# Optimization experiments

Hardware: AMD Instinct MI355X
Metric: run time of the kernel (lower is better)

## Reference

```python
import jax, jax.numpy as jnp
import numpy as np

B, S, D, H = 2, 2048, 1024, 16
HD = D // H  # 64


def setup_inputs() -> dict:
    key = jax.random.key(0)
    ks = jax.random.split(key, 11)
    w_scale = 1.0 / np.sqrt(D)
    Q = jax.random.normal(ks[0], (B, S, D), jnp.float32)
    K = jax.random.normal(ks[1], (B, S, D), jnp.float32)
    V = jax.random.normal(ks[2], (B, S, D), jnp.float32)
    # causal mask: True = masked (matches torch masked_fill semantics)
    mask = ~jnp.tril(jnp.ones((S, S), bool))[None, None]  # [1,1,S,S]
    # RoPE freqs (precomputed cos/sin of freqs_cis, shape [S, HD//2])
    inv_freq = 1.0 / (10000.0 ** (jnp.arange(0, HD, 2, dtype=jnp.float32) / HD))
    angles = jnp.arange(S, dtype=jnp.float32)[:, None] * inv_freq[None, :]
    freqs_cos, freqs_sin = jnp.cos(angles), jnp.sin(angles)
    wq = jax.random.normal(ks[3], (D, D), jnp.float32) * w_scale
    wk = jax.random.normal(ks[4], (D, D), jnp.float32) * w_scale
    wv = jax.random.normal(ks[5], (D, D), jnp.float32) * w_scale
    wo = jax.random.normal(ks[6], (D, D), jnp.float32) * w_scale
    bq = jax.random.normal(ks[7], (D,), jnp.float32) * 0.01
    bk = jax.random.normal(ks[8], (D,), jnp.float32) * 0.01
    bv = jax.random.normal(ks[9], (D,), jnp.float32) * 0.01
    bo = jax.random.normal(ks[10], (D,), jnp.float32) * 0.01
    return {"Q": Q, "K": K, "V": V, "mask": mask,
            "freqs_cos": freqs_cos, "freqs_sin": freqs_sin,
            "wq": wq, "bq": bq, "wk": wk, "bk": bk,
            "wv": wv, "bv": bv, "wo": wo, "bo": bo}


def _rope(x, cos, sin):
    # x: [B,S,H,HD]; complex pairing of adjacent dims as in view_as_complex
    xr, xi = x[..., 0::2], x[..., 1::2]
    c = cos[None, :, None, :]
    s = sin[None, :, None, :]
    out_r = xr * c - xi * s
    out_i = xr * s + xi * c
    return jnp.stack([out_r, out_i], axis=-1).reshape(x.shape)


def reference(Q, K, V, mask, freqs_cos, freqs_sin, wq, bq, wk, bk, wv, bv, wo, bo):
    b, s, d = Q.shape
    h = H
    hd = d // h
    q = (Q @ wq.T + bq).reshape(b, s, h, hd)
    k = (K @ wk.T + bk).reshape(b, s, h, hd)
    v = (V @ wv.T + bv).reshape(b, s, h, hd)
    q = _rope(q, freqs_cos, freqs_sin)
    k = _rope(k, freqs_cos, freqs_sin)
    q = q.transpose(0, 2, 1, 3)  # [B,H,S,HD]
    k = k.transpose(0, 2, 1, 3)
    v = v.transpose(0, 2, 1, 3)
    scale = jnp.sqrt(jnp.float32(hd))
    energy = jnp.einsum('bhqd,bhkd->bhqk', q, k) / scale
    energy = jnp.where(mask, jnp.float32(-1e10), energy)
    attn = jax.nn.softmax(energy, axis=-1)  # dropout p=0.0 -> identity
    out = jnp.einsum('bhqk,bhkd->bhqd', attn, v)
    out = out.transpose(0, 2, 1, 3).reshape(b, s, d)
    return out @ wo.T + bo
```

## Files before the change

### kernel.cpp

```cpp
#include <hip/hip_runtime.h>
#include <stdint.h>

#define NB 2
#define NS 2048
#define ND 1024
#define NH 16
#define NHD 64
#define NM (NB*NS)

typedef __bf16 bf16;
typedef float f32x4 __attribute__((ext_vector_type(4)));
typedef __bf16 bf16x8 __attribute__((ext_vector_type(8)));
typedef __bf16 bf16x4 __attribute__((ext_vector_type(4)));

#define MFMA16(a,b,c) __builtin_amdgcn_mfma_f32_16x16x32_bf16(a,b,c,0,0,0)

__device__ __forceinline__ void gld_lds16(const bf16* g, bf16* l) {
  __builtin_amdgcn_global_load_lds((const __attribute__((address_space(1))) void*)g,
                                   (__attribute__((address_space(3))) void*)l,
                                   16, 0, 0);
}

__device__ __forceinline__ void block_sync_lds() {
  asm volatile("s_waitcnt lgkmcnt(0)\n\ts_barrier" ::: "memory");
}

__global__ __launch_bounds__(256)
void cvt3(const float* __restrict__ s0, const float* __restrict__ s1,
          const float* __restrict__ s2, bf16* __restrict__ dst, int n4each) {
  const int t = blockIdx.y;
  const float* s = (t == 0) ? s0 : (t == 1) ? s1 : s2;
  int i = blockIdx.x * blockDim.x + threadIdx.x;
  if (i >= n4each) return;
  float4 v = ((const float4*)s)[i];
  bf16x4 o = { (bf16)v.x, (bf16)v.y, (bf16)v.z, (bf16)v.w };
  ((bf16x4*)(dst + (size_t)t * n4each * 4))[i] = o;
}

__global__ __launch_bounds__(256)
void cvt_w4(const float* __restrict__ s0, const float* __restrict__ s1,
            const float* __restrict__ s2, const float* __restrict__ s3,
            bf16* __restrict__ dst, int n4each) {
  const int t = blockIdx.y;
  const float* s = (t == 0) ? s0 : (t == 1) ? s1 : (t == 2) ? s2 : s3;
  int i = blockIdx.x * blockDim.x + threadIdx.x;
  if (i >= n4each) return;
  float4 v = ((const float4*)s)[i];
  bf16x4 o = { (bf16)v.x, (bf16)v.y, (bf16)v.z, (bf16)v.w };
  ((bf16x4*)(dst + (size_t)t * n4each * 4))[i] = o;
}

template<int MODE>
__global__ __launch_bounds__(256)
void gemm_nt(const bf16* __restrict__ A, const bf16* __restrict__ W,
             const float* __restrict__ b0, const float* __restrict__ b1,
             const float* __restrict__ b2,
             const float* __restrict__ fc, const float* __restrict__ fs,
             bf16* __restrict__ obf, float* __restrict__ of) {
  constexpr int K = ND;
  __shared__ __align__(16) bf16 As[128 * 32];
  __shared__ __align__(16) bf16 Bs[128 * 32];
  const int tid = threadIdx.x;
  const int w = tid >> 6, lane = tid & 63;
  const int nt = blockIdx.x, mt = blockIdx.y, t = blockIdx.z;
  const bf16* Ab = A + (size_t)t * ((size_t)NM * K);
  const bf16* Wb = W + (size_t)t * ((size_t)ND * K);
  const float* bias = (t == 0) ? b0 : (t == 1) ? b1 : b2;
  const int wr = (w >> 1) * 64, wc = (w & 1) * 64;
  f32x4 acc[4][4] = {};
  const bf16* ga = Ab + (size_t)(mt * 128 + (tid >> 2)) * K + (tid & 3) * 8;
  const bf16* gb = Wb + (size_t)(nt * 128 + (tid >> 2)) * K + (tid & 3) * 8;
  bf16* lA = As + w * 512;
  bf16* lB = Bs + w * 512;
  for (int k0 = 0; k0 < K; k0 += 32) {
    __syncthreads();
    gld_lds16(ga + k0, lA);
    gld_lds16(ga + (size_t)64 * K + k0, lA + 64 * 32);
    gld_lds16(gb + k0, lB);
    gld_lds16(gb + (size_t)64 * K + k0, lB + 64 * 32);
    __syncthreads();
    bf16x8 af[4], bfr[4];
#pragma unroll
    for (int i = 0; i < 4; ++i) {
      af[i]  = *(const bf16x8*)&As[(wr + i * 16 + (lane & 15)) * 32 + (lane >> 4) * 8];
      bfr[i] = *(const bf16x8*)&Bs[(wc + i * 16 + (lane & 15)) * 32 + (lane >> 4) * 8];
    }
#pragma unroll
    for (int i = 0; i < 4; ++i)
#pragma unroll
      for (int j = 0; j < 4; ++j)
        acc[i][j] = MFMA16(af[i], bfr[j], acc[i][j]);
  }
#pragma unroll
  for (int i = 0; i < 4; ++i) {
#pragma unroll
    for (int j = 0; j < 4; ++j) {
      const int gcol = nt * 128 + wc + j * 16 + (lane & 15);
      const float bv = bias[gcol];
#pragma unroll
      for (int r = 0; r < 4; ++r) {
        const int grow = mt * 128 + wr + i * 16 + (lane >> 4) * 4 + r;
        float v = acc[i][j][r] + bv;
        if (MODE == 0) {
          const int b = grow >> 11, s = grow & (NS - 1);
          const int h = gcol >> 6, hd = gcol & 63;
          if (t < 2) {
            float pv = __shfl_xor(v, 1);
            const int ii = hd >> 1;
            float c  = fc[(s << 5) + ii];
            float sn = fs[(s << 5) + ii];
            v = ((hd & 1) == 0) ? (v * c - pv * sn) : (pv * sn + v * c);
            if (t == 0) v *= 0.18033688011112042f;
          }
          obf[(size_t)t * ((size_t)NM * ND) +
              (((size_t)(b * NH + h) * NS + s) * NHD + hd)] = (bf16)v;
        } else {
          of[(size_t)grow * ND + gcol] = v;
        }
      }
    }
  }
}

__global__ __launch_bounds__(256)
void transpose_v(const bf16* __restrict__ v, bf16* __restrict__ vt) {
  __shared__ __align__(16) bf16 t[64][72];
  const int s0 = blockIdx.x * 64;
  const int bh = blockIdx.y;
  const bf16* src = v + ((size_t)bh * NS + s0) * NHD;
#pragma unroll
  for (int it = 0; it < 2; ++it) {
    int slot = threadIdx.x + it * 256;
    int r = slot >> 3, c8 = (slot & 7) * 8;
    *(bf16x8*)&t[r][c8] = *(const bf16x8*)&src[(size_t)r * NHD + c8];
  }
  __syncthreads();
  bf16* dst = vt + (size_t)bh * NHD * NS + s0;
#pragma unroll
  for (int it = 0; it < 2; ++it) {
    int slot = threadIdx.x + it * 256;
    int r = slot >> 3, c8 = (slot & 7) * 8;
    bf16x8 vv;
#pragma unroll
    for (int e = 0; e < 8; ++e) vv[e] = t[c8 + e][r];
    *(bf16x8*)&dst[(size_t)r * NS + c8] = vv;
  }
}

__device__ __forceinline__ void attn_tile(
    const bf16 (*__restrict__ Ksh)[72], const bf16 (*__restrict__ Vsh)[72],
    bf16 (*__restrict__ Pw)[72], const bf16x8* qf, f32x4* o,
    float& m, float& l, int qi, int kk0, bool diag, int qrow, int grp) {
  f32x4 sc[4] = {};
  __builtin_amdgcn_s_setprio(1);
#pragma unroll
  for (int ch = 0; ch < 2; ++ch)
#pragma unroll
    for (int cb = 0; cb < 4; ++cb) {
      bf16x8 kf = *(const bf16x8*)&Ksh[cb * 16 + qrow][ch * 32 + grp * 8];
      sc[cb] = MFMA16(kf, qf[ch], sc[cb]);
    }
  __builtin_amdgcn_s_setprio(0);

  if (diag) {
#pragma unroll
    for (int cb = 0; cb < 4; ++cb)
#pragma unroll
      for (int r = 0; r < 4; ++r)
        if (kk0 + cb * 16 + grp * 4 + r > qi) sc[cb][r] = -1e30f;
  }

  float pm = sc[0][0];
#pragma unroll
  for (int cb = 0; cb < 4; ++cb)
#pragma unroll
    for (int r = 0; r < 4; ++r) pm = fmaxf(pm, sc[cb][r]);
  pm = fmaxf(pm, __shfl_xor(pm, 16));
  pm = fmaxf(pm, __shfl_xor(pm, 32));
  const float mn = fmaxf(m, pm);
  const float scl = exp2f(m - mn);
  m = mn;
  l *= scl;
#pragma unroll
  for (int cb = 0; cb < 4; ++cb) {
    bf16x4 pk;
#pragma unroll
    for (int r = 0; r < 4; ++r) {
      float p = exp2f(sc[cb][r] - mn);
      l += p;
      pk[r] = (bf16)p;
    }
    *(bf16x4*)&Pw[qrow][cb * 16 + grp * 4] = pk;
  }
#pragma unroll
  for (int hb = 0; hb < 4; ++hb)
#pragma unroll
    for (int r = 0; r < 4; ++r) o[hb][r] *= scl;

  __builtin_amdgcn_s_setprio(1);
#pragma unroll
  for (int ch = 0; ch < 2; ++ch) {
    bf16x8 pa = *(const bf16x8*)&Pw[qrow][ch * 32 + grp * 8];
#pragma unroll
    for (int hb = 0; hb < 4; ++hb) {
      bf16x8 vf = *(const bf16x8*)&Vsh[hb * 16 + qrow][ch * 32 + grp * 8];
      o[hb] = MFMA16(vf, pa, o[hb]);
    }
  }
  __builtin_amdgcn_s_setprio(0);
}

__global__ __launch_bounds__(512, 4)
void attn_k(const bf16* __restrict__ q, const bf16* __restrict__ k,
            const bf16* __restrict__ vt, bf16* __restrict__ out) {
  __shared__ __align__(16) char smem[55296];
  auto Ks = (bf16(*)[64][72])smem;
  auto Vs = (bf16(*)[64][72])(smem + 18432);
  auto P  = (bf16(*)[16][72])(smem + 36864);
  auto MO = (float(*)[2][16][68])smem;
  auto ML = (float(*)[2][16][2])(smem + 36864);

  const int tid = threadIdx.x;
  const int w = tid >> 6, lane = tid & 63;
  const int h = w >> 2, wl = w & 3;
  const int qrow = lane & 15, grp = lane >> 4;
  const int bh = blockIdx.x, j = blockIdx.y;
  const int b = bh >> 4, hh = bh & (NH - 1);
  const int tA = j, tB = 31 - j;

  const bf16* qb = q + (size_t)bh * NS * NHD;
  const bf16* kb = k + (size_t)bh * NS * NHD;
  const bf16* vb = vt + (size_t)bh * NHD * NS;

  const int nA = (j >= h) ? (((j - h) >> 1) + 1) : 0;
  const int nB = (((31 - j) - h) >> 1) + 1;
  const int len = nA + nB;

  const int q0A = tA * 64 + wl * 16, q0B = tB * 64 + wl * 16;
  bf16x8 qfA[2], qfB[2];
#pragma unroll
  for (int ch = 0; ch < 2; ++ch) {
    qfA[ch] = *(const bf16x8*)&qb[(size_t)(q0A + qrow) * NHD + ch * 32 + grp * 8];
    qfB[ch] = *(const bf16x8*)&qb[(size_t)(q0B + qrow) * NHD + ch * 32 + grp * 8];
  }

  f32x4 oA[4] = {}, oB[4] = {};
  float mA = -1e30f, lA = 0.f, mB = -1e30f, lB = 0.f;

  const int local = tid & 255;
  const int r0 = local >> 3, c0 = (local & 7) * 8;

  bf16x8 ka0, ka1, va0, va1;
  auto load_round = [&](int r) {
    const bool isA = r < nA;
    const int kt = isA ? (h + 2 * r) : (h + 2 * (r - nA));
    const int kk0 = kt * 64;
    ka0 = *(const bf16x8*)&kb[(size_t)(kk0 + r0) * NHD + c0];
    ka1 = *(const bf16x8*)&kb[(size_t)(kk0 + r0 + 32) * NHD + c0];
    va0 = *(const bf16x8*)&vb[(size_t)r0 * NS + kk0 + c0];
    va1 = *(const bf16x8*)&vb[(size_t)(r0 + 32) * NS + kk0 + c0];
  };

  load_round(0);
  for (int r = 0; r < 17; ++r) {
    const bool act = r < len;
    if (act) {
      *(bf16x8*)&Ks[h][r0][c0]      = ka0;
      *(bf16x8*)&Ks[h][r0 + 32][c0] = ka1;
      *(bf16x8*)&Vs[h][r0][c0]      = va0;
      *(bf16x8*)&Vs[h][r0 + 32][c0] = va1;
    }
    block_sync_lds();
    const bool isA = r < nA;
    const int kt = isA ? (h + 2 * r) : (h + 2 * (r - nA));
    if (r + 1 < len) load_round(r + 1);
    if (act) {
      if (isA)
        attn_tile(Ks[h], Vs[h], P[w], qfA, oA, mA, lA,
                  q0A + qrow, kt * 64, kt == tA, qrow, grp);
      else
        attn_tile(Ks[h], Vs[h], P[w], qfB, oB, mB, lB,
                  q0B + qrow, kt * 64, kt == tB, qrow, grp);
    }
    block_sync_lds();
  }

  lA += __shfl_xor(lA, 16); lA += __shfl_xor(lA, 32);
  lB += __shfl_xor(lB, 16); lB += __shfl_xor(lB, 32);

  __syncthreads();

  if (h == 1) {
#pragma unroll
    for (int hb = 0; hb < 4; ++hb) {
      *(f32x4*)&MO[wl][0][qrow][hb * 16 + grp * 4] = oA[hb];
      *(f32x4*)&MO[wl][1][qrow][hb * 16 + grp * 4] = oB[hb];
    }
    if (grp == 0) {
      ML[wl][0][qrow][0] = mA; ML[wl][0][qrow][1] = lA;
      ML[wl][1][qrow][0] = mB; ML[wl][1][qrow][1] = lB;
    }
  }
  __syncthreads();

  if (h == 0) {
#pragma unroll
    for (int sub = 0; sub < 2; ++sub) {
      const float m0 = sub ? mB : mA, l0 = sub ? lB : lA;
      const f32x4* o0 = sub ? oB : oA;
      const float m1 = ML[wl][sub][qrow][0], l1 = ML[wl][sub][qrow][1];
      const float mm = fmaxf(m0, m1);
      const float s0 = exp2f(m0 - mm), s1 = exp2f(m1 - mm);
      const float inv = 1.f / (l0 * s0 + l1 * s1);
      const int s = (sub ? q0B : q0A) + qrow;
      bf16* op = out + (size_t)(b * NS + s) * ND + hh * NHD + grp * 4;
#pragma unroll
      for (int hb = 0; hb < 4; ++hb) {
        f32x4 o1 = *(const f32x4*)&MO[wl][sub][qrow][hb * 16 + grp * 4];
        bf16x4 ov = { (bf16)((o0[hb][0] * s0 + o1[0] * s1) * inv),
                      (bf16)((o0[hb][1] * s0 + o1[1] * s1) * inv),
                      (bf16)((o0[hb][2] * s0 + o1[2] * s1) * inv),
                      (bf16)((o0[hb][3] * s0 + o1[3] * s1) * inv) };
        *(bf16x4*)&op[hb * 16] = ov;
      }
    }
  }
}

extern "C" void kernel_launch(void* const* d_in, const int* in_sizes, int n_in,
                              void* d_out, int out_size, void* d_ws, size_t ws_size,
                              hipStream_t stream) {
  const float* Q  = (const float*)d_in[0];
  const float* K  = (const float*)d_in[1];
  const float* V  = (const float*)d_in[2];
  const float* fc = (const float*)d_in[4];
  const float* fs = (const float*)d_in[5];
  const float* wq = (const float*)d_in[6];
  const float* bq = (const float*)d_in[7];
  const float* wk = (const float*)d_in[8];
  const float* bk = (const float*)d_in[9];
  const float* wv = (const float*)d_in[10];
  const float* bv = (const float*)d_in[11];
  const float* wo = (const float*)d_in[12];
  const float* bo = (const float*)d_in[13];
  float* out = (float*)d_out;
  bf16* ws = (bf16*)d_ws;

  const size_t MB_ = 1024 * 1024;
  bf16* Qbf  = ws;
  bf16* Wqkv = ws + 12 * MB_;
  bf16* Wo   = ws + 15 * MB_;
  bf16* qp   = ws + 16 * MB_;
  bf16* kp   = ws + 20 * MB_;
  bf16* vp   = ws + 24 * MB_;
  bf16* vtp  = ws + 28 * MB_;
  bf16* aout = ws + 32 * MB_;

  cvt3<<<dim3(4096, 3), 256, 0, stream>>>(Q, K, V, Qbf, 1048576);
  cvt_w4<<<dim3(1024, 4), 256, 0, stream>>>(wq, wk, wv, wo, Wqkv, 262144);

  gemm_nt<0><<<dim3(8, 32, 3), 256, 0, stream>>>(Qbf, Wqkv, bq, bk, bv, fc, fs, qp, nullptr);

  transpose_v<<<dim3(32, 32), 256, 0, stream>>>(vp, vtp);

  attn_k<<<dim3(32, 16), 512, 0, stream>>>(qp, kp, vtp, aout);

  gemm_nt<1><<<dim3(8, 32, 1), 256, 0, stream>>>(aout, Wo, bo, bo, bo, fc, fs, nullptr, out);
}
```

Before: 144.1 us.

## Double-buffer GEMM LDS loads, remap blocks per XCD, narrow output-projection tile

The GEMM kernel now double-buffers its LDS tiles and issues the next k-slice's global-to-LDS loads before computing the current one. Partial vmcnt waits let memory traffic overlap the MFMA work. Blocks are launched on a 1D grid and remapped so that consecutive IDs on the same XCD share M-tiles, which is meant to improve L2 reuse. The output projection uses a 64-wide N tile, giving 512 blocks instead of 256 to fill more CUs, at the cost of doubled LDS use and fewer MFMAs per load.

```diff
diff --git a/kernel.cpp b/kernel.cpp
--- a/kernel.cpp
+++ b/kernel.cpp
@@ -58,49 +58,80 @@
              const float* __restrict__ fc, const float* __restrict__ fs,
              bf16* __restrict__ obf, float* __restrict__ of) {
   constexpr int K = ND;
-  __shared__ __align__(16) bf16 As[128 * 32];
-  __shared__ __align__(16) bf16 Bs[128 * 32];
+  constexpr int BN = (MODE == 0) ? 128 : 64;
+  constexpr int NJ = (MODE == 0) ? 4 : 2;
+  __shared__ __align__(16) bf16 As[2][128 * 32];
+  __shared__ __align__(16) bf16 Bs[2][BN * 32];
   const int tid = threadIdx.x;
   const int w = tid >> 6, lane = tid & 63;
-  const int nt = blockIdx.x, mt = blockIdx.y, t = blockIdx.z;
+
+  const int id = blockIdx.x;
+  const int xcd = id & 7, r = id >> 3;
+  int t, nt, mt;
+  if (MODE == 0) { t = r >> 5; const int rem = r & 31; nt = rem & 7;  mt = xcd + 8 * (rem >> 3); }
+  else           { t = 0;                              nt = r & 15;   mt = xcd + 8 * (r >> 4);   }
+
   const bf16* Ab = A + (size_t)t * ((size_t)NM * K);
   const bf16* Wb = W + (size_t)t * ((size_t)ND * K);
   const float* bias = (t == 0) ? b0 : (t == 1) ? b1 : b2;
-  const int wr = (w >> 1) * 64, wc = (w & 1) * 64;
-  f32x4 acc[4][4] = {};
+  const int wr = (w >> 1) * 64, wc = (w & 1) * (BN / 2);
+  f32x4 acc[4][NJ] = {};
   const bf16* ga = Ab + (size_t)(mt * 128 + (tid >> 2)) * K + (tid & 3) * 8;
-  const bf16* gb = Wb + (size_t)(nt * 128 + (tid >> 2)) * K + (tid & 3) * 8;
-  bf16* lA = As + w * 512;
-  bf16* lB = Bs + w * 512;
+  const bf16* gb = Wb + (size_t)(nt * BN + (tid >> 2)) * K + (tid & 3) * 8;
+  bf16* lA = (bf16*)As + w * 512;
+  bf16* lB = (bf16*)Bs + w * 512;
+
+  auto issue = [&](int k0, int buf) {
+    gld_lds16(ga + k0, lA + buf * (128 * 32));
+    gld_lds16(ga + (size_t)64 * K + k0, lA + buf * (128 * 32) + 64 * 32);
+    if (MODE == 0) {
+      gld_lds16(gb + k0, lB + buf * (BN * 32));
+      gld_lds16(gb + (size_t)64 * K + k0, lB + buf * (BN * 32) + 64 * 32);
+    } else {
+      gld_lds16(gb + k0, lB + buf * (BN * 32));
+    }
+  };
+
+  issue(0, 0);
+  int cur = 0;
   for (int k0 = 0; k0 < K; k0 += 32) {
-    __syncthreads();
-    gld_lds16(ga + k0, lA);
-    gld_lds16(ga + (size_t)64 * K + k0, lA + 64 * 32);
-    gld_lds16(gb + k0, lB);
-    gld_lds16(gb + (size_t)64 * K + k0, lB + 64 * 32);
-    __syncthreads();
-    bf16x8 af[4], bfr[4];
-#pragma unroll
-    for (int i = 0; i < 4; ++i) {
-      af[i]  = *(const bf16x8*)&As[(wr + i * 16 + (lane & 15)) * 32 + (lane >> 4) * 8];
-      bfr[i] = *(const bf16x8*)&Bs[(wc + i * 16 + (lane & 15)) * 32 + (lane >> 4) * 8];
-    }
+    const bool last = (k0 + 32 >= K);
+    if (!last) {
+      issue(k0 + 32, cur ^ 1);
+      if (MODE == 0) asm volatile("s_waitcnt vmcnt(4)" ::: "memory");
+      else           asm volatile("s_waitcnt vmcnt(3)" ::: "memory");
+    } else {
+      asm volatile("s_waitcnt vmcnt(0)" ::: "memory");
+    }
+    __builtin_amdgcn_s_barrier();
+
+    bf16x8 af[4], bfr[NJ];
 #pragma unroll
     for (int i = 0; i < 4; ++i)
-#pragma unroll
-      for (int j = 0; j < 4; ++j)
+      af[i] = *(const bf16x8*)&As[cur][(wr + i * 16 + (lane & 15)) * 32 + (lane >> 4) * 8];
+#pragma unroll
+    for (int j = 0; j < NJ; ++j)
+      bfr[j] = *(const bf16x8*)&Bs[cur][(wc + j * 16 + (lane & 15)) * 32 + (lane >> 4) * 8];
+#pragma unroll
+    for (int i = 0; i < 4; ++i)
+#pragma unroll
+      for (int j = 0; j < NJ; ++j)
         acc[i][j] = MFMA16(af[i], bfr[j], acc[i][j]);
-  }
+
+    block_sync_lds();
+    cur ^= 1;
+  }
+
 #pragma unroll
   for (int i = 0; i < 4; ++i) {
 #pragma unroll
-    for (int j = 0; j < 4; ++j) {
-      const int gcol = nt * 128 + wc + j * 16 + (lane & 15);
+    for (int j = 0; j < NJ; ++j) {
+      const int gcol = nt * BN + wc + j * 16 + (lane & 15);
       const float bv = bias[gcol];
 #pragma unroll
-      for (int r = 0; r < 4; ++r) {
-        const int grow = mt * 128 + wr + i * 16 + (lane >> 4) * 4 + r;
-        float v = acc[i][j][r] + bv;
+      for (int r4 = 0; r4 < 4; ++r4) {
+        const int grow = mt * 128 + wr + i * 16 + (lane >> 4) * 4 + r4;
+        float v = acc[i][j][r4] + bv;
         if (MODE == 0) {
           const int b = grow >> 11, s = grow & (NS - 1);
           const int h = gcol >> 6, hd = gcol & 63;
@@ -359,11 +390,11 @@
   cvt3<<<dim3(4096, 3), 256, 0, stream>>>(Q, K, V, Qbf, 1048576);
   cvt_w4<<<dim3(1024, 4), 256, 0, stream>>>(wq, wk, wv, wo, Wqkv, 262144);
 
-  gemm_nt<0><<<dim3(8, 32, 3), 256, 0, stream>>>(Qbf, Wqkv, bq, bk, bv, fc, fs, qp, nullptr);
+  gemm_nt<0><<<768, 256, 0, stream>>>(Qbf, Wqkv, bq, bk, bv, fc, fs, qp, nullptr);
 
   transpose_v<<<dim3(32, 32), 256, 0, stream>>>(vp, vtp);
 
   attn_k<<<dim3(32, 16), 512, 0, stream>>>(qp, kp, vtp, aout);
 
-  gemm_nt<1><<<dim3(8, 32, 1), 256, 0, stream>>>(aout, Wo, bo, bo, bo, fc, fs, nullptr, out);
-}
+  gemm_nt<1><<<512, 256, 0, stream>>>(aout, Wo, bo, bo, bo, fc, fs, nullptr, out);
+}
```

Measured after the change: 150.0 us. 4.1% more time.
